# Kernel tuning notes

Measured on AMD Instinct MI355X. Metric: run time of the kernel, lower is better.

Reference implementation:

```python
import jax, jax.numpy as jnp
import numpy as np

NUM_HEADS = 8
AREA = 4
EPS = 1e-5  # torch BatchNorm2d default


def _conv1x1(x, w):
    # x: [B,C,H,W], w: [O,C] -> [B,O,H,W]
    return jnp.einsum('bchw,oc->bohw', x, w)


def _bn(y, g, b, m, v):
    # inference-mode BatchNorm2d, per-channel affine
    s = g / jnp.sqrt(v + EPS)
    return y * s[None, :, None, None] + (b - m * s)[None, :, None, None]


def setup_inputs() -> dict:
    key = jax.random.key(0)
    ks = jax.random.split(key, 16)
    B, C, H, W = 2, 256, 64, 64
    d = {}
    d['x'] = jax.random.normal(ks[0], (B, C, H, W), jnp.float32)
    # qk conv (dim -> 2*dim) + BN
    d['w_qk'] = jax.random.normal(ks[1], (2 * C, C), jnp.float32) * 0.06
    d['g_qk'] = jax.random.uniform(ks[2], (2 * C,), jnp.float32, 0.5, 1.5)
    d['b_qk'] = jax.random.normal(ks[3], (2 * C,), jnp.float32) * 0.1
    d['m_qk'] = jax.random.normal(ks[4], (2 * C,), jnp.float32) * 0.1
    d['v_qk'] = jax.random.uniform(ks[5], (2 * C,), jnp.float32, 0.5, 1.5)
    # v conv (dim -> dim) + BN
    d['w_v'] = jax.random.normal(ks[6], (C, C), jnp.float32) * 0.06
    d['g_v'] = jax.random.uniform(ks[7], (C,), jnp.float32, 0.5, 1.5)
    d['b_v'] = jax.random.normal(ks[8], (C,), jnp.float32) * 0.1
    d['m_v'] = jax.random.normal(ks[9], (C,), jnp.float32) * 0.1
    d['v_v'] = jax.random.uniform(ks[10], (C,), jnp.float32, 0.5, 1.5)
    # proj conv (dim -> dim) + BN
    d['w_p'] = jax.random.normal(ks[11], (C, C), jnp.float32) * 0.06
    d['g_p'] = jax.random.uniform(ks[12], (C,), jnp.float32, 0.5, 1.5)
    d['b_p'] = jax.random.normal(ks[13], (C,), jnp.float32) * 0.1
    d['m_p'] = jax.random.normal(ks[14], (C,), jnp.float32) * 0.1
    d['v_p'] = jax.random.uniform(ks[15], (C,), jnp.float32, 0.5, 1.5)
    return d


def reference(x, w_qk, g_qk, b_qk, m_qk, v_qk,
              w_v, g_v, b_v, m_v, v_v,
              w_p, g_p, b_p, m_p, v_p):
    B, C, H, W = x.shape
    N = H * W
    hd = C // NUM_HEADS

    qk = _bn(_conv1x1(x, w_qk), g_qk, b_qk, m_qk, v_qk)          # [B,2C,H,W]
    qk = qk.reshape(B, 2 * C, N).transpose(0, 2, 1)               # [B,N,2C]
    vv = _bn(_conv1x1(x, w_v), g_v, b_v, m_v, v_v)                # [B,C,H,W]
    vv = vv.reshape(B, C, N).transpose(0, 2, 1)                   # [B,N,C]

    Ba, Na = B * AREA, N // AREA
    qk = qk.reshape(Ba, Na, 2 * C)
    vv = vv.reshape(Ba, Na, C)
    q, k = qk[..., :C], qk[..., C:]

    # [Ba,Na,C] -> [Ba,heads,hd,Na] (matches torch transpose(1,2).view)
    q = q.reshape(Ba, Na, NUM_HEADS, hd).transpose(0, 2, 3, 1)
    k = k.reshape(Ba, Na, NUM_HEADS, hd).transpose(0, 2, 3, 1)
    v = vv.reshape(Ba, Na, NUM_HEADS, hd).transpose(0, 2, 3, 1)

    scale = hd ** -0.5
    attn = jnp.einsum('bhdi,bhdj->bhij', q, k) * scale            # [Ba,h,Na,Na]
    attn = jax.nn.softmax(attn, axis=-1)                          # max-sub exp/sum
    out = jnp.einsum('bhdj,bhij->bihd', v, attn)                  # [Ba,Na,h,hd]

    out = out.reshape(B, N, C).reshape(B, H, W, C).transpose(0, 3, 1, 2)
    return _bn(_conv1x1(out, w_p), g_p, b_p, m_p, v_p)            # [B,C,H,W]
```

## Files before the change

kernel.cpp:

```cpp
#include <hip/hip_runtime.h>
#include <hip/hip_bf16.h>
#include <math.h>

#define CCH   256
#define NPIX  4096
#define NHD   8
#define HD    32
#define NA    1024
#define BN_EPS 1e-5f
#define ATT_SCALE (0.17677669529663687f * 1.4426950408889634f)

typedef __attribute__((ext_vector_type(8))) short bf16x8;
typedef __attribute__((ext_vector_type(4))) short bf16x4;
typedef __attribute__((ext_vector_type(4))) float f32x4;

static __device__ inline short f2bf(float f) {
    union { float f; unsigned u; } v; v.f = f;
    unsigned r = (v.u + 0x7fff + ((v.u >> 16) & 1)) >> 16;
    return (short)r;
}

static __device__ inline unsigned int pk2bf(float a, float b) {
    __hip_bfloat162 h2 = __float22bfloat162_rn(make_float2(a, b));
    union { __hip_bfloat162 h; unsigned int u; } v; v.h = h2;
    return v.u;
}

__global__ __launch_bounds__(256)
void prep_kernel(const float* __restrict__ x, short* __restrict__ Xt,
                 const float* __restrict__ wqk, const float* __restrict__ wv,
                 const float* __restrict__ wp, short* __restrict__ Wb) {
    __shared__ short tile[64][66];
    const int t = threadIdx.x;
    const int z = blockIdx.z;
    if (z == 2) {
        const int id  = blockIdx.y * 64 + blockIdx.x;
        const int idx = (id * 256 + t) * 4;
        const float* src; int off;
        if (idx < 131072)      { src = wqk; off = idx; }
        else if (idx < 196608) { src = wv;  off = idx - 131072; }
        else                   { src = wp;  off = idx - 196608; }
        const float4 v = *(const float4*)(src + off);
        short4 o;
        o.x = f2bf(v.x); o.y = f2bf(v.y); o.z = f2bf(v.z); o.w = f2bf(v.w);
        *(short4*)(Wb + idx) = o;
        return;
    }
    const int n0 = blockIdx.x << 6;
    const int c0 = blockIdx.y << 6;
    const int b  = z;
    const float* xp = x + (((size_t)(b * CCH + c0)) << 12) + n0;
    #pragma unroll
    for (int j = 0; j < 16; ++j) {
        const int lin = (j << 8) + t;
        const int cl = lin >> 6, nl = lin & 63;
        tile[cl][nl] = f2bf(xp[((size_t)cl << 12) + nl]);
    }
    __syncthreads();
    short* xtp = Xt + ((((size_t)b << 12) + n0) << 8) + c0;
    #pragma unroll
    for (int j = 0; j < 16; ++j) {
        const int lin = (j << 8) + t;
        const int nl = lin >> 6, cl = lin & 63;
        xtp[((size_t)nl << 8) + cl] = tile[cl][nl];
    }
}

__global__ __launch_bounds__(256)
void qkv_gemm(const short* __restrict__ Xt, const short* __restrict__ Wb,
              const float* __restrict__ g_qk, const float* __restrict__ b_qk,
              const float* __restrict__ m_qk, const float* __restrict__ v_qk,
              const float* __restrict__ g_v, const float* __restrict__ b_v,
              const float* __restrict__ m_v, const float* __restrict__ v_v,
              short* __restrict__ Qb, short* __restrict__ Kb,
              short* __restrict__ Vb) {
    const int lane = threadIdx.x & 63;
    const int w    = threadIdx.x >> 6;
    const int c    = lane & 15;
    const int quad = lane >> 4;
    const int m0 = blockIdx.x * 64 + (w >> 1) * 32;
    const int n0 = blockIdx.y * 128 + (w & 1) * 64;

    const short* ap = Xt + ((size_t)(m0 + c) << 8) + (quad << 3);
    const short* bp = Wb + ((size_t)(n0 + c) << 8) + (quad << 3);

    f32x4 acc[2][4];
    #pragma unroll
    for (int f = 0; f < 2; ++f)
        #pragma unroll
        for (int g = 0; g < 4; ++g) acc[f][g] = (f32x4){0.f, 0.f, 0.f, 0.f};

    #pragma unroll
    for (int k = 0; k < 256; k += 32) {
        bf16x8 af[2], bg[4];
        #pragma unroll
        for (int f = 0; f < 2; ++f) af[f] = *(const bf16x8*)(ap + f * 4096 + k);
        #pragma unroll
        for (int g = 0; g < 4; ++g) bg[g] = *(const bf16x8*)(bp + g * 4096 + k);
        #pragma unroll
        for (int f = 0; f < 2; ++f)
            #pragma unroll
            for (int g = 0; g < 4; ++g)
                acc[f][g] = __builtin_amdgcn_mfma_f32_16x16x32_bf16(af[f], bg[g], acc[f][g], 0, 0, 0);
    }

    if (n0 < 512) {
        const bool isQ = (n0 < 256);
        short* dst = isQ ? Qb : Kb;
        const float fold = isQ ? ATT_SCALE : 1.0f;
        #pragma unroll
        for (int g = 0; g < 4; ++g) {
            const int o  = n0 + g * 16 + c;
            const int cd = o & 255;
            const int h  = cd >> 5;
            const int d  = cd & 31;
            float s    = g_qk[o] * rsqrtf(v_qk[o] + BN_EPS);
            float beta = (b_qk[o] - m_qk[o] * s) * fold;
            s *= fold;
            #pragma unroll
            for (int f = 0; f < 2; ++f) {
                #pragma unroll
                for (int r = 0; r < 4; ++r) {
                    const int row  = m0 + f * 16 + (quad << 2) + r;
                    const int pair = (row >> 10) * NHD + h;
                    const int i    = row & 1023;
                    dst[(((size_t)pair << 10) + i) * HD + d] = f2bf(acc[f][g][r] * s + beta);
                }
            }
        }
    } else {
        #pragma unroll
        for (int g = 0; g < 4; ++g) {
            const int c2 = n0 + g * 16 + c - 512;
            const int d  = c2 & 31;
            const int hp = c2 >> 5;
            const float s    = g_v[c2] * rsqrtf(v_v[c2] + BN_EPS);
            const float beta = b_v[c2] - m_v[c2] * s;
            #pragma unroll
            for (int f = 0; f < 2; ++f) {
                #pragma unroll
                for (int r = 0; r < 4; ++r) {
                    const int row  = m0 + f * 16 + (quad << 2) + r;
                    const int pair = (row >> 10) * NHD + hp;
                    const int j    = row & 1023;
                    Vb[((size_t)pair << 15) + (d << 10) + j] = f2bf(acc[f][g][r] * s + beta);
                }
            }
        }
    }
}

__global__ __launch_bounds__(256, 4)
void attn_kernel(const short* __restrict__ Qb,
                 const short* __restrict__ Kb,
                 const short* __restrict__ Vb,
                 short* __restrict__ AOt) {
    const int tid  = threadIdx.x;
    const int wave = tid >> 6;
    const int lane = tid & 63;
    const int c    = lane & 15;
    const int quad = lane >> 4;
    const int pidx  = wave >> 1;
    const int jhalf = wave & 1;

    const int bx  = blockIdx.x;
    const int hi  = bx >> 3;
    const int p   = (bx & 7) + ((hi >> 4) << 3);
    const int blk = hi & 15;
    const int i0a = (blk << 6) + (pidx << 5);
    const int i0b = i0a + 16;
    const int ba  = p >> 3;
    const int h   = p & 7;

    __shared__ f32x4 mrgA[2][4][64];
    __shared__ float mrgL[2][2][64];

    const short* qbase = Qb + ((size_t)p << 15);
    const short* kbase = Kb + ((size_t)p << 15);
    const short* vbase = Vb + ((size_t)p << 15);

    bf16x8 qfa = *(const bf16x8*)(qbase + ((i0a + c) << 5) + (quad << 3));
    bf16x8 qfb = *(const bf16x8*)(qbase + ((i0b + c) << 5) + (quad << 3));

    const int perm = ((c >> 2) << 3) + (c & 3);
    const short* kp0 = kbase + (perm << 5) + (quad << 3);
    const short* kp1 = kp0 + 128;
    const short* vp0 = vbase + (c << 10) + (quad << 3);
    const short* vp1 = vbase + ((c + 16) << 10) + (quad << 3);

    f32x4 acc0a = {0.f,0.f,0.f,0.f}, acc1a = {0.f,0.f,0.f,0.f};
    f32x4 acc0b = {0.f,0.f,0.f,0.f}, acc1b = {0.f,0.f,0.f,0.f};
    float la = 0.f, lb = 0.f;
    const f32x4 zero = {0.f,0.f,0.f,0.f};

    const int jbeg = jhalf << 9;
    for (int jj = 0; jj < 512; jj += 32) {
        const int j0 = jbeg + jj;
        bf16x8 kf0 = *(const bf16x8*)(kp0 + (j0 << 5));
        bf16x8 kf1 = *(const bf16x8*)(kp1 + (j0 << 5));
        bf16x8 vf0 = *(const bf16x8*)(vp0 + j0);
        bf16x8 vf1 = *(const bf16x8*)(vp1 + j0);

        f32x4 s0a = __builtin_amdgcn_mfma_f32_16x16x32_bf16(kf0, qfa, zero, 0, 0, 0);
        f32x4 s1a = __builtin_amdgcn_mfma_f32_16x16x32_bf16(kf1, qfa, zero, 0, 0, 0);
        f32x4 s0b = __builtin_amdgcn_mfma_f32_16x16x32_bf16(kf0, qfb, zero, 0, 0, 0);
        f32x4 s1b = __builtin_amdgcn_mfma_f32_16x16x32_bf16(kf1, qfb, zero, 0, 0, 0);

        float p0a[4], p1a[4], p0b[4], p1b[4];
        #pragma unroll
        for (int r = 0; r < 4; ++r) {
            p0a[r] = __builtin_amdgcn_exp2f(s0a[r]);
            p1a[r] = __builtin_amdgcn_exp2f(s1a[r]);
            p0b[r] = __builtin_amdgcn_exp2f(s0b[r]);
            p1b[r] = __builtin_amdgcn_exp2f(s1b[r]);
        }
        la += (p0a[0]+p0a[1]) + (p0a[2]+p0a[3]) + (p1a[0]+p1a[1]) + (p1a[2]+p1a[3]);
        lb += (p0b[0]+p0b[1]) + (p0b[2]+p0b[3]) + (p1b[0]+p1b[1]) + (p1b[2]+p1b[3]);

        union { unsigned int u[4]; bf16x8 v; } pfa, pfb;
        pfa.u[0] = pk2bf(p0a[0], p0a[1]);
        pfa.u[1] = pk2bf(p0a[2], p0a[3]);
        pfa.u[2] = pk2bf(p1a[0], p1a[1]);
        pfa.u[3] = pk2bf(p1a[2], p1a[3]);
        pfb.u[0] = pk2bf(p0b[0], p0b[1]);
        pfb.u[1] = pk2bf(p0b[2], p0b[3]);
        pfb.u[2] = pk2bf(p1b[0], p1b[1]);
        pfb.u[3] = pk2bf(p1b[2], p1b[3]);

        acc0a = __builtin_amdgcn_mfma_f32_16x16x32_bf16(pfa.v, vf0, acc0a, 0, 0, 0);
        acc1a = __builtin_amdgcn_mfma_f32_16x16x32_bf16(pfa.v, vf1, acc1a, 0, 0, 0);
        acc0b = __builtin_amdgcn_mfma_f32_16x16x32_bf16(pfb.v, vf0, acc0b, 0, 0, 0);
        acc1b = __builtin_amdgcn_mfma_f32_16x16x32_bf16(pfb.v, vf1, acc1b, 0, 0, 0);
    }

    if (jhalf == 1) {
        mrgA[pidx][0][lane] = acc0a;
        mrgA[pidx][1][lane] = acc1a;
        mrgA[pidx][2][lane] = acc0b;
        mrgA[pidx][3][lane] = acc1b;
        mrgL[pidx][0][lane] = la;
        mrgL[pidx][1][lane] = lb;
    }
    __syncthreads();
    if (jhalf == 1) return;

    acc0a += mrgA[pidx][0][lane];
    acc1a += mrgA[pidx][1][lane];
    acc0b += mrgA[pidx][2][lane];
    acc1b += mrgA[pidx][3][lane];
    la += mrgL[pidx][0][lane];
    lb += mrgL[pidx][1][lane];

    la += __shfl_xor(la, 16); la += __shfl_xor(la, 32);
    lb += __shfl_xor(lb, 16); lb += __shfl_xor(lb, 32);

    #pragma unroll
    for (int r = 0; r < 4; ++r) {
        const int rr = (quad << 2) + r;
        const float rla = 1.f / __shfl(la, rr, 16);
        const float rlb = 1.f / __shfl(lb, rr, 16);
        const size_t basea = ((((size_t)ba << 10) + i0a + rr) << 8) + (h << 5);
        const size_t baseb = ((((size_t)ba << 10) + i0b + rr) << 8) + (h << 5);
        AOt[basea + c]      = f2bf(acc0a[r] * rla);
        AOt[basea + c + 16] = f2bf(acc1a[r] * rla);
        AOt[baseb + c]      = f2bf(acc0b[r] * rlb);
        AOt[baseb + c + 16] = f2bf(acc1b[r] * rlb);
    }
}

__global__ __launch_bounds__(256)
void pconv_gemm(const short* __restrict__ Wp, const short* __restrict__ AOt,
                const float* __restrict__ g_p, const float* __restrict__ b_p,
                const float* __restrict__ m_p, const float* __restrict__ v_p,
                float* __restrict__ out) {
    const int lane = threadIdx.x & 63;
    const int w    = threadIdx.x >> 6;
    const int c    = lane & 15;
    const int quad = lane >> 4;
    const int m0 = blockIdx.x * 64 + (w >> 1) * 32;
    const int n0 = blockIdx.y * 128 + (w & 1) * 64;

    const short* ap = Wp + ((size_t)(m0 + c) << 8) + (quad << 3);
    const short* bp = AOt + ((size_t)(n0 + c) << 8) + (quad << 3);

    f32x4 acc[2][4];
    #pragma unroll
    for (int f = 0; f < 2; ++f)
        #pragma unroll
        for (int g = 0; g < 4; ++g) acc[f][g] = (f32x4){0.f, 0.f, 0.f, 0.f};

    #pragma unroll
    for (int k = 0; k < 256; k += 32) {
        bf16x8 af[2], bg[4];
        #pragma unroll
        for (int f = 0; f < 2; ++f) af[f] = *(const bf16x8*)(ap + f * 4096 + k);
        #pragma unroll
        for (int g = 0; g < 4; ++g) bg[g] = *(const bf16x8*)(bp + g * 4096 + k);
        #pragma unroll
        for (int f = 0; f < 2; ++f)
            #pragma unroll
            for (int g = 0; g < 4; ++g)
                acc[f][g] = __builtin_amdgcn_mfma_f32_16x16x32_bf16(af[f], bg[g], acc[f][g], 0, 0, 0);
    }

    #pragma unroll
    for (int f = 0; f < 2; ++f) {
        #pragma unroll
        for (int r = 0; r < 4; ++r) {
            const int o = m0 + f * 16 + (quad << 2) + r;
            const float s    = g_p[o] * rsqrtf(v_p[o] + BN_EPS);
            const float beta = b_p[o] - m_p[o] * s;
            #pragma unroll
            for (int g = 0; g < 4; ++g) {
                const int col = n0 + g * 16 + c;
                const int b = col >> 12, n = col & 4095;
                out[((size_t)(b * CCH + o) << 12) + n] = acc[f][g][r] * s + beta;
            }
        }
    }
}

extern "C" void kernel_launch(void* const* d_in, const int* in_sizes, int n_in,
                              void* d_out, int out_size, void* d_ws, size_t ws_size,
                              hipStream_t stream) {
    const float* x    = (const float*)d_in[0];
    const float* w_qk = (const float*)d_in[1];
    const float* g_qk = (const float*)d_in[2];
    const float* b_qk = (const float*)d_in[3];
    const float* m_qk = (const float*)d_in[4];
    const float* v_qk = (const float*)d_in[5];
    const float* w_v  = (const float*)d_in[6];
    const float* g_v  = (const float*)d_in[7];
    const float* b_v  = (const float*)d_in[8];
    const float* m_v  = (const float*)d_in[9];
    const float* v_v  = (const float*)d_in[10];
    const float* w_p  = (const float*)d_in[11];
    const float* g_p  = (const float*)d_in[12];
    const float* b_p  = (const float*)d_in[13];
    const float* m_p  = (const float*)d_in[14];
    const float* v_p  = (const float*)d_in[15];

    short* Qb  = (short*)d_ws;
    short* Kb  = Qb + 2097152;
    short* Vb  = Kb + 2097152;
    short* Xt  = Vb + 2097152;
    short* Wb  = Xt + 2097152;
    short* AOt = Xt;

    dim3 gprep(64, 4, 3);
    prep_kernel<<<gprep, 256, 0, stream>>>(x, Xt, w_qk, w_v, w_p, Wb);

    dim3 gqkv(128, 6);
    qkv_gemm<<<gqkv, 256, 0, stream>>>(Xt, Wb, g_qk, b_qk, m_qk, v_qk,
                                       g_v, b_v, m_v, v_v, Qb, Kb, Vb);

    attn_kernel<<<1024, 256, 0, stream>>>(Qb, Kb, Vb, AOt);

    dim3 gp(4, 64);
    pconv_gemm<<<gp, 256, 0, stream>>>(Wb + 768 * 256, AOt, g_p, b_p, m_p, v_p, (float*)d_out);
}
```

Measured before the change: 145.6 us.

## Stage GEMM operand tiles through padded LDS with 64x64 block tiles

The qkv and projection GEMMs now load 64x64 K-chunks of A and B cooperatively into padded shared memory, and the MFMA fragments are read from LDS instead of each wave loading directly from global memory. Block tiles shrink from 64x128 to 64x64, so each wave computes 32x32 and the grids double, which raises block count and occupancy. This aims to coalesce global loads and cut redundant operand fetches. The cost is extra barriers and LDS traffic without double buffering, plus less register reuse per wave.

```diff
diff --git a/kernel.cpp b/kernel.cpp
--- a/kernel.cpp
+++ b/kernel.cpp
@@ -74,43 +74,71 @@
               const float* __restrict__ m_v, const float* __restrict__ v_v,
               short* __restrict__ Qb, short* __restrict__ Kb,
               short* __restrict__ Vb) {
-    const int lane = threadIdx.x & 63;
-    const int w    = threadIdx.x >> 6;
+    __shared__ short A_lds[64][72];
+    __shared__ short B_lds[64][72];
+    const int t    = threadIdx.x;
+    const int lane = t & 63;
+    const int w    = t >> 6;
     const int c    = lane & 15;
     const int quad = lane >> 4;
-    const int m0 = blockIdx.x * 64 + (w >> 1) * 32;
-    const int n0 = blockIdx.y * 128 + (w & 1) * 64;
-
-    const short* ap = Xt + ((size_t)(m0 + c) << 8) + (quad << 3);
-    const short* bp = Wb + ((size_t)(n0 + c) << 8) + (quad << 3);
-
-    f32x4 acc[2][4];
+    const int wm   = w >> 1;
+    const int wn   = w & 1;
+    const int m0 = blockIdx.x * 64;
+    const int n0 = blockIdx.y * 64;
+
+    const int rowS = t >> 3;
+    const int kc   = t & 7;
+    const short* gA0 = Xt + (size_t)(m0 + rowS) * 256 + kc * 8;
+    const short* gA1 = gA0 + 32 * 256;
+    const short* gB0 = Wb + (size_t)(n0 + rowS) * 256 + kc * 8;
+    const short* gB1 = gB0 + 32 * 256;
+    short* lA0 = &A_lds[rowS][kc * 8];
+    short* lA1 = &A_lds[rowS + 32][kc * 8];
+    short* lB0 = &B_lds[rowS][kc * 8];
+    short* lB1 = &B_lds[rowS + 32][kc * 8];
+
+    f32x4 acc[2][2];
     #pragma unroll
     for (int f = 0; f < 2; ++f)
         #pragma unroll
-        for (int g = 0; g < 4; ++g) acc[f][g] = (f32x4){0.f, 0.f, 0.f, 0.f};
-
-    #pragma unroll
-    for (int k = 0; k < 256; k += 32) {
-        bf16x8 af[2], bg[4];
-        #pragma unroll
-        for (int f = 0; f < 2; ++f) af[f] = *(const bf16x8*)(ap + f * 4096 + k);
-        #pragma unroll
-        for (int g = 0; g < 4; ++g) bg[g] = *(const bf16x8*)(bp + g * 4096 + k);
-        #pragma unroll
-        for (int f = 0; f < 2; ++f)
-            #pragma unroll
-            for (int g = 0; g < 4; ++g)
-                acc[f][g] = __builtin_amdgcn_mfma_f32_16x16x32_bf16(af[f], bg[g], acc[f][g], 0, 0, 0);
-    }
-
+        for (int g = 0; g < 2; ++g) acc[f][g] = (f32x4){0.f, 0.f, 0.f, 0.f};
+
+    #pragma unroll
+    for (int kt = 0; kt < 4; ++kt) {
+        const int k0 = kt * 64;
+        bf16x8 a0 = *(const bf16x8*)(gA0 + k0);
+        bf16x8 a1 = *(const bf16x8*)(gA1 + k0);
+        bf16x8 b0 = *(const bf16x8*)(gB0 + k0);
+        bf16x8 b1 = *(const bf16x8*)(gB1 + k0);
+        if (kt) __syncthreads();
+        *(bf16x8*)lA0 = a0;
+        *(bf16x8*)lA1 = a1;
+        *(bf16x8*)lB0 = b0;
+        *(bf16x8*)lB1 = b1;
+        __syncthreads();
+        #pragma unroll
+        for (int s = 0; s < 2; ++s) {
+            const int ko = s * 32 + quad * 8;
+            bf16x8 af0 = *(const bf16x8*)&A_lds[wm * 32 + c][ko];
+            bf16x8 af1 = *(const bf16x8*)&A_lds[wm * 32 + 16 + c][ko];
+            bf16x8 bg0 = *(const bf16x8*)&B_lds[wn * 32 + c][ko];
+            bf16x8 bg1 = *(const bf16x8*)&B_lds[wn * 32 + 16 + c][ko];
+            acc[0][0] = __builtin_amdgcn_mfma_f32_16x16x32_bf16(af0, bg0, acc[0][0], 0, 0, 0);
+            acc[0][1] = __builtin_amdgcn_mfma_f32_16x16x32_bf16(af0, bg1, acc[0][1], 0, 0, 0);
+            acc[1][0] = __builtin_amdgcn_mfma_f32_16x16x32_bf16(af1, bg0, acc[1][0], 0, 0, 0);
+            acc[1][1] = __builtin_amdgcn_mfma_f32_16x16x32_bf16(af1, bg1, acc[1][1], 0, 0, 0);
+        }
+    }
+
+    const int mw = m0 + wm * 32;
+    const int nw = n0 + wn * 32;
     if (n0 < 512) {
         const bool isQ = (n0 < 256);
         short* dst = isQ ? Qb : Kb;
         const float fold = isQ ? ATT_SCALE : 1.0f;
         #pragma unroll
-        for (int g = 0; g < 4; ++g) {
-            const int o  = n0 + g * 16 + c;
+        for (int g = 0; g < 2; ++g) {
+            const int o  = nw + g * 16 + c;
             const int cd = o & 255;
             const int h  = cd >> 5;
             const int d  = cd & 31;
@@ -121,7 +149,7 @@
             for (int f = 0; f < 2; ++f) {
                 #pragma unroll
                 for (int r = 0; r < 4; ++r) {
-                    const int row  = m0 + f * 16 + (quad << 2) + r;
+                    const int row  = mw + f * 16 + (quad << 2) + r;
                     const int pair = (row >> 10) * NHD + h;
                     const int i    = row & 1023;
                     dst[(((size_t)pair << 10) + i) * HD + d] = f2bf(acc[f][g][r] * s + beta);
@@ -130,8 +158,8 @@
         }
     } else {
         #pragma unroll
-        for (int g = 0; g < 4; ++g) {
-            const int c2 = n0 + g * 16 + c - 512;
+        for (int g = 0; g < 2; ++g) {
+            const int c2 = nw + g * 16 + c - 512;
             const int d  = c2 & 31;
             const int hp = c2 >> 5;
             const float s    = g_v[c2] * rsqrtf(v_v[c2] + BN_EPS);
@@ -140,7 +168,7 @@
             for (int f = 0; f < 2; ++f) {
                 #pragma unroll
                 for (int r = 0; r < 4; ++r) {
-                    const int row  = m0 + f * 16 + (quad << 2) + r;
+                    const int row  = mw + f * 16 + (quad << 2) + r;
                     const int pair = (row >> 10) * NHD + hp;
                     const int j    = row & 1023;
                     Vb[((size_t)pair << 15) + (d << 10) + j] = f2bf(acc[f][g][r] * s + beta);
@@ -273,46 +301,74 @@
                 const float* __restrict__ g_p, const float* __restrict__ b_p,
                 const float* __restrict__ m_p, const float* __restrict__ v_p,
                 float* __restrict__ out) {
-    const int lane = threadIdx.x & 63;
-    const int w    = threadIdx.x >> 6;
+    __shared__ short A_lds[64][72];
+    __shared__ short B_lds[64][72];
+    const int t    = threadIdx.x;
+    const int lane = t & 63;
+    const int w    = t >> 6;
     const int c    = lane & 15;
     const int quad = lane >> 4;
-    const int m0 = blockIdx.x * 64 + (w >> 1) * 32;
-    const int n0 = blockIdx.y * 128 + (w & 1) * 64;
-
-    const short* ap = Wp + ((size_t)(m0 + c) << 8) + (quad << 3);
-    const short* bp = AOt + ((size_t)(n0 + c) << 8) + (quad << 3);
-
-    f32x4 acc[2][4];
+    const int wm   = w >> 1;
+    const int wn   = w & 1;
+    const int m0 = blockIdx.x * 64;
+    const int n0 = blockIdx.y * 64;
+
+    const int rowS = t >> 3;
+    const int kc   = t & 7;
+    const short* gA0 = Wp + (size_t)(m0 + rowS) * 256 + kc * 8;
+    const short* gA1 = gA0 + 32 * 256;
+    const short* gB0 = AOt + (size_t)(n0 + rowS) * 256 + kc * 8;
+    const short* gB1 = gB0 + 32 * 256;
+    short* lA0 = &A_lds[rowS][kc * 8];
+    short* lA1 = &A_lds[rowS + 32][kc * 8];
+    short* lB0 = &B_lds[rowS][kc * 8];
+    short* lB1 = &B_lds[rowS + 32][kc * 8];
+
+    f32x4 acc[2][2];
     #pragma unroll
     for (int f = 0; f < 2; ++f)
         #pragma unroll
-        for (int g = 0; g < 4; ++g) acc[f][g] = (f32x4){0.f, 0.f, 0.f, 0.f};
-
-    #pragma unroll
-    for (int k = 0; k < 256; k += 32) {
-        bf16x8 af[2], bg[4];
-        #pragma unroll
-        for (int f = 0; f < 2; ++f) af[f] = *(const bf16x8*)(ap + f * 4096 + k);
-        #pragma unroll
-        for (int g = 0; g < 4; ++g) bg[g] = *(const bf16x8*)(bp + g * 4096 + k);
-        #pragma unroll
-        for (int f = 0; f < 2; ++f)
-            #pragma unroll
-            for (int g = 0; g < 4; ++g)
-                acc[f][g] = __builtin_amdgcn_mfma_f32_16x16x32_bf16(af[f], bg[g], acc[f][g], 0, 0, 0);
-    }
-
+        for (int g = 0; g < 2; ++g) acc[f][g] = (f32x4){0.f, 0.f, 0.f, 0.f};
+
+    #pragma unroll
+    for (int kt = 0; kt < 4; ++kt) {
+        const int k0 = kt * 64;
+        bf16x8 a0 = *(const bf16x8*)(gA0 + k0);
+        bf16x8 a1 = *(const bf16x8*)(gA1 + k0);
+        bf16x8 b0 = *(const bf16x8*)(gB0 + k0);
+        bf16x8 b1 = *(const bf16x8*)(gB1 + k0);
+        if (kt) __syncthreads();
+        *(bf16x8*)lA0 = a0;
+        *(bf16x8*)lA1 = a1;
+        *(bf16x8*)lB0 = b0;
+        *(bf16x8*)lB1 = b1;
+        __syncthreads();
+        #pragma unroll
+        for (int s = 0; s < 2; ++s) {
+            const int ko = s * 32 + quad * 8;
+            bf16x8 af0 = *(const bf16x8*)&A_lds[wm * 32 + c][ko];
+            bf16x8 af1 = *(const bf16x8*)&A_lds[wm * 32 + 16 + c][ko];
+            bf16x8 bg0 = *(const bf16x8*)&B_lds[wn * 32 + c][ko];
+            bf16x8 bg1 = *(const bf16x8*)&B_lds[wn * 32 + 16 + c][ko];
+            acc[0][0] = __builtin_amdgcn_mfma_f32_16x16x32_bf16(af0, bg0, acc[0][0], 0, 0, 0);
+            acc[0][1] = __builtin_amdgcn_mfma_f32_16x16x32_bf16(af0, bg1, acc[0][1], 0, 0, 0);
+            acc[1][0] = __builtin_amdgcn_mfma_f32_16x16x32_bf16(af1, bg0, acc[1][0], 0, 0, 0);
+            acc[1][1] = __builtin_amdgcn_mfma_f32_16x16x32_bf16(af1, bg1, acc[1][1], 0, 0, 0);
+        }
+    }
+
+    const int mw = m0 + wm * 32;
+    const int nw = n0 + wn * 32;
     #pragma unroll
     for (int f = 0; f < 2; ++f) {
         #pragma unroll
         for (int r = 0; r < 4; ++r) {
-            const int o = m0 + f * 16 + (quad << 2) + r;
+            const int o = mw + f * 16 + (quad << 2) + r;
             const float s    = g_p[o] * rsqrtf(v_p[o] + BN_EPS);
             const float beta = b_p[o] - m_p[o] * s;
             #pragma unroll
-            for (int g = 0; g < 4; ++g) {
-                const int col = n0 + g * 16 + c;
+            for (int g = 0; g < 2; ++g) {
+                const int col = nw + g * 16 + c;
                 const int b = col >> 12, n = col & 4095;
                 out[((size_t)(b * CCH + o) << 12) + n] = acc[f][g][r] * s + beta;
             }
@@ -350,12 +406,12 @@
     dim3 gprep(64, 4, 3);
     prep_kernel<<<gprep, 256, 0, stream>>>(x, Xt, w_qk, w_v, w_p, Wb);
 
-    dim3 gqkv(128, 6);
+    dim3 gqkv(128, 12);
     qkv_gemm<<<gqkv, 256, 0, stream>>>(Xt, Wb, g_qk, b_qk, m_qk, v_qk,
                                        g_v, b_v, m_v, v_v, Qb, Kb, Vb);
 
     attn_kernel<<<1024, 256, 0, stream>>>(Qb, Kb, Vb, AOt);
 
-    dim3 gp(4, 64);
+    dim3 gp(4, 128);
     pconv_gemm<<<gp, 256, 0, stream>>>(Wb + 768 * 256, AOt, g_p, b_p, m_p, v_p, (float*)d_out);
 }
```

Result: faster. 132.1 us (-9.3%).
